# Performance work log

Hardware: AMD Instinct MI355X
Metric: run time of the kernel (lower is better)

The kernel has to match this reference:

```python
import jax, jax.numpy as jnp
import numpy as np
from jax import lax

B, N, FEAT, MID, HID, OUT = 128, 36, 2048, 517, 128, 1024
STEPS, TEMP = 3, 1.0


def setup_inputs() -> dict:
    key = jax.random.key(0)
    ks = jax.random.split(key, 10)
    s = 0.02
    return {
        "boxes": jax.random.uniform(ks[0], (B, 4, N), jnp.float32),
        "attention": jax.random.normal(ks[1], (B, N), jnp.float32),
        "features": jax.random.normal(ks[2], (B, N, FEAT), jnp.float32),
        "conv_w": jax.random.normal(ks[3], (MID - 5, FEAT), jnp.float32) * s,
        "conv_b": jnp.zeros((MID - 5,), jnp.float32),
        "skew_wx": jax.random.normal(ks[4], (HID, MID), jnp.float32) * s,
        "skew_wy": jax.random.normal(ks[5], (HID, MID), jnp.float32) * s,
        "skew_b1": jnp.zeros((HID,), jnp.float32),
        "skew_w2": jax.random.normal(ks[6], (HID,), jnp.float32) * s,
        "skew_b2": jnp.zeros((1,), jnp.float32),
        "w_ih": jax.random.normal(ks[7], (4 * OUT, MID), jnp.float32) * s,
        "w_hh": jax.random.normal(ks[8], (4 * OUT, OUT), jnp.float32) * s,
        "b_ih": jnp.zeros((4 * OUT,), jnp.float32),
        "b_hh": jnp.zeros((4 * OUT,), jnp.float32),
        "lr": jnp.ones((1,), jnp.float32),
    }


def _calculate_assignment(C, lr_abs, temp, steps):
    # C: (b, n, n) skew-symmetric ordering costs.
    logits = jnp.zeros_like(C)
    for _ in range(steps):
        P = jax.nn.softmax(logits / temp, axis=-1)  # position i -> distribution over elements l
        cum = jnp.cumsum(P, axis=1)                 # sum over positions k <= i
        below = cum - P                             # sum_{k<i} P_kl
        above = cum[:, -1:, :] - cum                # sum_{k>i} P_kl
        # grad_{ij} = sum_l C_{jl} * (above - below)_{il}  (uses skew-symmetry of C)
        G = jnp.einsum('bil,bjl->bij', above - below, C)
        logits = logits - lr_abs * G
    return jax.nn.softmax(logits / temp, axis=-1)


def reference(boxes, attention, features, conv_w, conv_b, skew_wx, skew_wy,
              skew_b1, skew_w2, skew_b2, w_ih, w_hh, b_ih, b_hh, lr):
    b = boxes.shape[0]
    # normalize boxes by per-sample max
    boxes = boxes / jnp.max(boxes.reshape(b, -1), axis=1)[:, None, None]
    # pointwise Conv1: 2048 -> MID-5, features arrives as (b, n, 2048)
    f = jnp.einsum('bnf,mf->bmn', features, conv_w) + conv_b[None, :, None]
    att = attention[:, None, :]                      # (b, 1, n)
    feats = jnp.concatenate([boxes, att, f], axis=1)  # (b, MID, n)
    # PairwiseSkew: f(x_i, x_j) - f(x_j, x_i); the first 1x1-conv over concatenated
    # pairs splits into two linear maps so we never materialize (b, 2*MID, n, n).
    hx = jnp.einsum('hm,bmn->bhn', skew_wx, feats)
    hy = jnp.einsum('hm,bmn->bhn', skew_wy, feats)
    h = jax.nn.relu(hx[:, :, :, None] + hy[:, :, None, :] + skew_b1[None, :, None, None])
    out = jnp.einsum('h,bhij->bij', skew_w2, h) + skew_b2[0]  # (b, n, n)
    C = out - jnp.swapaxes(out, 1, 2)  # skew-symmetrize
    A = _calculate_assignment(C, jnp.abs(lr)[0], TEMP, STEPS)
    # gate features by sigmoid(attention) and apply soft permutation
    gated = feats * jax.nn.sigmoid(att)               # (b, MID, n)
    x = jnp.einsum('bcl,bil->bci', gated, A)          # (b, MID, n)
    x_seq = jnp.transpose(x, (2, 0, 1))               # (n, b, MID)
    # single-layer LSTM (PyTorch gate order i, f, g, o); return final cell state
    bias = b_ih + b_hh
    Hd = w_hh.shape[1]
    def step(carry, xt):
        h_, c_ = carry
        gates = xt @ w_ih.T + h_ @ w_hh.T + bias
        i, fg, g, o = jnp.split(gates, 4, axis=-1)
        c_ = jax.nn.sigmoid(fg) * c_ + jax.nn.sigmoid(i) * jnp.tanh(g)
        h_ = jax.nn.sigmoid(o) * jnp.tanh(c_)
        return (h_, c_), None
    init = (jnp.zeros((b, Hd), x.dtype), jnp.zeros((b, Hd), x.dtype))
    (_, c_fin), _ = lax.scan(step, init, x_seq)
    return c_fin
```

## Files before the change

### kernel.cpp

```cpp
#include <hip/hip_runtime.h>
#include <math.h>

#define NB 128
#define NN 36
#define S37 37
#define S40 40
#define NFEAT 2048
#define NMID 517
#define KP 544
#define NHID 128
#define NOUT 1024
#define ROWS (NB*NN)

typedef __bf16 bf16x8 __attribute__((ext_vector_type(8)));
typedef float  f32x4  __attribute__((ext_vector_type(4)));

__device__ __forceinline__ float sigf(float x){ return 1.f/(1.f+expf(-x)); }
__device__ __forceinline__ unsigned short f2bf(float x){
    unsigned u = __float_as_uint(x);
    return (unsigned short)((u + 0x7FFFu + ((u>>16)&1u)) >> 16);
}
__device__ __forceinline__ float bf2f(unsigned short b){
    return __uint_as_float(((unsigned)b) << 16);
}

__global__ __launch_bounds__(256) void prep_all(
    const float* __restrict__ boxes, const float* __restrict__ att,
    const float* __restrict__ features, const float* __restrict__ conv_w,
    const float* __restrict__ wx, const float* __restrict__ wy,
    const float* __restrict__ b1, const float* __restrict__ w_ih,
    const float* __restrict__ w_hh, const float* __restrict__ b_ih,
    const float* __restrict__ b_hh,
    unsigned short* __restrict__ features_bf, unsigned short* __restrict__ convw_bf,
    unsigned short* __restrict__ wxy_bf, float* __restrict__ hxy_b,
    unsigned short* __restrict__ wih_il, unsigned short* __restrict__ whh_il,
    float* __restrict__ comb_b, unsigned short* __restrict__ h0,
    float* __restrict__ c, float* __restrict__ feats)
{
    int gtid = blockIdx.x*256 + threadIdx.x;
    int gs = gridDim.x*256;
    if (gtid < 128*64) {
        int b = gtid >> 6, t = gtid & 63;
        float mx = -1e30f;
        for (int idx = t; idx < 4*NN; idx += 64) mx = fmaxf(mx, boxes[b*4*NN + idx]);
        for (int off = 32; off > 0; off >>= 1) mx = fmaxf(mx, __shfl_down(mx, off));
        mx = __shfl(mx, 0);
        float inv = 1.f / mx;
        for (int idx = t; idx < 4*NN; idx += 64) {
            int r = idx / NN, n = idx - r*NN;
            feats[(size_t)(b*NN+n)*NMID + r] = boxes[b*4*NN + idx] * inv;
        }
        if (t < NN) feats[(size_t)(b*NN+t)*NMID + 4] = att[b*NN + t];
    }
    for (int i = gtid; i < ROWS*NFEAT; i += gs) features_bf[i] = f2bf(features[i]);
    for (int i = gtid; i < 512*NFEAT; i += gs) convw_bf[i] = f2bf(conv_w[i]);
    for (int i = gtid; i < 256*KP; i += gs) {
        int r = i / KP, k = i - r*KP;
        float v = 0.f;
        if (k < NMID) v = (r < NHID) ? wx[(size_t)r*NMID+k] : wy[(size_t)(r-NHID)*NMID+k];
        wxy_bf[i] = f2bf(v);
    }
    for (int i = gtid; i < 256; i += gs) hxy_b[i] = (i < NHID) ? b1[i] : 0.f;
    for (int i = gtid; i < 4*NOUT*KP; i += gs) {
        int row = i / KP, k = i - row*KP;
        int u = row >> 2, g = row & 3;
        wih_il[i] = (k < NMID) ? f2bf(w_ih[(size_t)(g*NOUT+u)*NMID + k]) : (unsigned short)0;
    }
    for (int i = gtid; i < 4*NOUT*NOUT; i += gs) {
        int row = i >> 10, k = i & 1023;
        int u = row >> 2, g = row & 3;
        whh_il[i] = f2bf(w_hh[(size_t)(g*NOUT+u)*NOUT + k]);
    }
    for (int i = gtid; i < 4*NOUT; i += gs) {
        int u = i >> 2, g = i & 3;
        comb_b[i] = b_ih[g*NOUT+u] + b_hh[g*NOUT+u];
    }
    for (int i = gtid; i < NB*NOUT; i += gs) { h0[i] = 0; c[i] = 0.f; }
}

__global__ __launch_bounds__(256) void conv_sk(
    const unsigned short* __restrict__ A, const unsigned short* __restrict__ B,
    float* __restrict__ part)
{
    __shared__ __align__(16) char As[8192];
    __shared__ __align__(16) char Bs[4096];
    int m0 = blockIdx.y * 128, n0 = blockIdx.x * 64;
    int kbeg = blockIdx.z * 512;
    int tid = threadIdx.x;
    int lane = tid & 63, wave = tid >> 6;
    int wm = wave >> 1, wn = wave & 1;
    f32x4 acc[4][2];
    #pragma unroll
    for (int i = 0; i < 4; ++i)
        #pragma unroll
        for (int j = 0; j < 2; ++j) acc[i][j] = (f32x4){0.f,0.f,0.f,0.f};

    for (int k0 = 0; k0 < 512; k0 += 32) {
        #pragma unroll
        for (int cc = tid; cc < 512; cc += 256) {
            int r = cc >> 2, q = cc & 3;
            uint4 v = *(const uint4*)(A + (size_t)(m0+r)*NFEAT + kbeg + k0 + q*8);
            *(uint4*)(As + ((r>>4)<<10) + (q<<8) + ((r&15)<<4)) = v;
        }
        {
            int r = tid >> 2, q = tid & 3;
            uint4 v = *(const uint4*)(B + (size_t)(n0+r)*NFEAT + kbeg + k0 + q*8);
            *(uint4*)(Bs + ((r>>4)<<10) + (q<<8) + ((r&15)<<4)) = v;
        }
        __syncthreads();
        bf16x8 af[4], bfr[2];
        #pragma unroll
        for (int i = 0; i < 4; ++i) af[i]  = *(bf16x8*)(As + ((wm*4+i)<<10) + (lane<<4));
        #pragma unroll
        for (int j = 0; j < 2; ++j) bfr[j] = *(bf16x8*)(Bs + ((wn*2+j)<<10) + (lane<<4));
        #pragma unroll
        for (int i = 0; i < 4; ++i)
            #pragma unroll
            for (int j = 0; j < 2; ++j)
                acc[i][j] = __builtin_amdgcn_mfma_f32_16x16x32_bf16(af[i], bfr[j], acc[i][j], 0, 0, 0);
        __syncthreads();
    }
    float* out = part + (size_t)blockIdx.z * ROWS * 512;
    int colf = lane & 15, rowq = lane >> 4;
    #pragma unroll
    for (int j = 0; j < 2; ++j) {
        int col = n0 + (wn*2+j)*16 + colf;
        #pragma unroll
        for (int i = 0; i < 4; ++i)
            #pragma unroll
            for (int reg = 0; reg < 4; ++reg) {
                int row = m0 + (wm*4+i)*16 + rowq*4 + reg;
                out[(size_t)row*512 + col] = acc[i][j][reg];
            }
    }
}

__global__ __launch_bounds__(256) void conv_reduce(
    const float* __restrict__ part, const float* __restrict__ bias,
    float* __restrict__ feats, unsigned short* __restrict__ feats_bf)
{
    int gtid = blockIdx.x*256 + threadIdx.x;
    int gs = gridDim.x*256;
    const size_t PS = (size_t)ROWS * 512;
    for (int i = gtid; i < ROWS*512; i += gs) {
        int r = i >> 9, cc = i & 511;
        float s = part[i] + part[PS+i] + part[2*PS+i] + part[3*PS+i] + bias[cc];
        feats[(size_t)r*NMID + 5 + cc] = s;
        feats_bf[(size_t)r*KP + 5 + cc] = f2bf(s);
    }
    for (int i = gtid; i < ROWS*5; i += gs) {
        int r = i / 5, cc = i - r*5;
        feats_bf[(size_t)r*KP + cc] = f2bf(feats[(size_t)r*NMID + cc]);
    }
    for (int i = gtid; i < ROWS*27; i += gs) {
        int r = i / 27, cc = i - r*27;
        feats_bf[(size_t)r*KP + 517 + cc] = 0;
    }
}

__global__ __launch_bounds__(256) void gemm_mfma(
    const unsigned short* __restrict__ A, const unsigned short* __restrict__ B,
    const float* __restrict__ bias, void* __restrict__ Cp,
    int K, int lda, int ldb, int ldc, int obf)
{
    __shared__ __align__(16) char As[8192];
    __shared__ __align__(16) char Bs[4096];
    int m0 = blockIdx.y * 128, n0 = blockIdx.x * 64;
    int tid = threadIdx.x;
    int lane = tid & 63, wave = tid >> 6;
    int wm = wave >> 1, wn = wave & 1;
    f32x4 acc[4][2];
    #pragma unroll
    for (int i = 0; i < 4; ++i)
        #pragma unroll
        for (int j = 0; j < 2; ++j) acc[i][j] = (f32x4){0.f,0.f,0.f,0.f};

    for (int k0 = 0; k0 < K; k0 += 32) {
        #pragma unroll
        for (int cc = tid; cc < 512; cc += 256) {
            int r = cc >> 2, q = cc & 3;
            uint4 v = *(const uint4*)(A + (size_t)(m0+r)*lda + k0 + q*8);
            *(uint4*)(As + ((r>>4)<<10) + (q<<8) + ((r&15)<<4)) = v;
        }
        {
            int r = tid >> 2, q = tid & 3;
            uint4 v = *(const uint4*)(B + (size_t)(n0+r)*ldb + k0 + q*8);
            *(uint4*)(Bs + ((r>>4)<<10) + (q<<8) + ((r&15)<<4)) = v;
        }
        __syncthreads();
        bf16x8 af[4], bfr[2];
        #pragma unroll
        for (int i = 0; i < 4; ++i) af[i]  = *(bf16x8*)(As + ((wm*4+i)<<10) + (lane<<4));
        #pragma unroll
        for (int j = 0; j < 2; ++j) bfr[j] = *(bf16x8*)(Bs + ((wn*2+j)<<10) + (lane<<4));
        #pragma unroll
        for (int i = 0; i < 4; ++i)
            #pragma unroll
            for (int j = 0; j < 2; ++j)
                acc[i][j] = __builtin_amdgcn_mfma_f32_16x16x32_bf16(af[i], bfr[j], acc[i][j], 0, 0, 0);
        __syncthreads();
    }
    int colf = lane & 15, rowq = lane >> 4;
    #pragma unroll
    for (int j = 0; j < 2; ++j) {
        int col = n0 + (wn*2+j)*16 + colf;
        float bv = bias ? bias[col] : 0.f;
        #pragma unroll
        for (int i = 0; i < 4; ++i) {
            #pragma unroll
            for (int reg = 0; reg < 4; ++reg) {
                int row = m0 + (wm*4+i)*16 + rowq*4 + reg;
                float v = acc[i][j][reg] + bv;
                if (obf) ((unsigned short*)Cp)[(size_t)row*ldc + col] = f2bf(v);
                else     ((float*)Cp)[(size_t)row*ldc + col] = v;
            }
        }
    }
}

__global__ __launch_bounds__(256) void out_k(
    const float* __restrict__ hxy, const float* __restrict__ w2,
    float* __restrict__ out_g)
{
    __shared__ float s_hx[9*129], s_hy[NN*129], s_w2[NHID];
    int b = blockIdx.x, i0 = blockIdx.y * 9, tid = threadIdx.x;
    for (int i = tid; i < 9*NHID; i += 256) {
        int n = i >> 7, h = i & 127;
        s_hx[n*129+h] = hxy[(size_t)(b*NN+i0+n)*256 + h];
    }
    for (int i = tid; i < NN*NHID; i += 256) {
        int n = i >> 7, h = i & 127;
        s_hy[n*129+h] = hxy[(size_t)(b*NN+n)*256 + 128 + h];
    }
    if (tid < NHID) s_w2[tid] = w2[tid];
    __syncthreads();
    for (int idx = tid; idx < 9*NN; idx += 256) {
        int il = idx / NN, j = idx - il*NN;
        const float* px = &s_hx[il*129];
        const float* py = &s_hy[j*129];
        float s = 0.f;
        #pragma unroll 8
        for (int h = 0; h < NHID; ++h) s += s_w2[h] * fmaxf(px[h] + py[h], 0.f);
        out_g[(size_t)b*NN*NN + (i0+il)*NN + j] = s;
    }
}

__global__ __launch_bounds__(256) void iter_k(
    const float* __restrict__ out_g, const float* __restrict__ att,
    const float* __restrict__ lr, float* __restrict__ A_g)
{
    __shared__ __align__(16) float s_out[NN*S40], s_C[NN*S40], s_logits[NN*S40], s_P[NN*S40];
    __shared__ float s_sg[NN];
    int b = blockIdx.x, tid = threadIdx.x;
    for (int idx = tid; idx < NN*NN; idx += 256) {
        int i = idx / NN, j = idx - i*NN;
        s_out[i*S40+j] = out_g[(size_t)b*NN*NN + idx];
        s_logits[i*S40+j] = 0.f;
    }
    if (tid < NN) s_sg[tid] = sigf(att[b*NN + tid]);
    float lr_abs = fabsf(lr[0]);
    __syncthreads();
    for (int idx = tid; idx < NN*NN; idx += 256) {
        int i = idx / NN, j = idx - i*NN;
        s_C[i*S40+j] = s_out[i*S40+j] - s_out[j*S40+i];
    }
    __syncthreads();
    for (int it = 0; it < 3; ++it) {
        if (tid < NN) {
            int i = tid;
            float mx = -1e30f;
            for (int l = 0; l < NN; ++l) mx = fmaxf(mx, s_logits[i*S40+l]);
            float sum = 0.f;
            for (int l = 0; l < NN; ++l) { float e = expf(s_logits[i*S40+l]-mx); s_P[i*S40+l] = e; sum += e; }
            float inv = 1.f/sum;
            for (int l = 0; l < NN; ++l) s_P[i*S40+l] *= inv;
        }
        __syncthreads();
        if (tid < NN) {
            int l = tid;
            float S = 0.f;
            for (int i = 0; i < NN; ++i) S += s_P[i*S40+l];
            float cum = 0.f;
            for (int i = 0; i < NN; ++i) {
                float p = s_P[i*S40+l];
                cum += p;
                s_P[i*S40+l] = S - 2.f*cum + p;
            }
        }
        __syncthreads();
        for (int idx = tid; idx < NN*NN; idx += 256) {
            int i = idx / NN, j = idx - i*NN;
            const f32x4* Pp = (const f32x4*)&s_P[i*S40];
            const f32x4* Cc = (const f32x4*)&s_C[j*S40];
            float g = 0.f;
            #pragma unroll
            for (int q = 0; q < 9; ++q) {
                f32x4 a = Pp[q], bb = Cc[q];
                g += a[0]*bb[0] + a[1]*bb[1] + a[2]*bb[2] + a[3]*bb[3];
            }
            s_logits[i*S40+j] -= lr_abs * g;
        }
        __syncthreads();
    }
    if (tid < NN) {
        int i = tid;
        float mx = -1e30f;
        for (int l = 0; l < NN; ++l) mx = fmaxf(mx, s_logits[i*S40+l]);
        float sum = 0.f;
        for (int l = 0; l < NN; ++l) { float e = expf(s_logits[i*S40+l]-mx); s_P[i*S40+l] = e; sum += e; }
        float inv = 1.f/sum;
        for (int l = 0; l < NN; ++l)
            A_g[(size_t)b*NN*NN + i*NN + l] = s_P[i*S40+l] * inv * s_sg[l];
    }
}

__global__ __launch_bounds__(256) void xseq_k(
    const float* __restrict__ feats, const float* __restrict__ A_g,
    unsigned short* __restrict__ xseq)
{
    __shared__ float s_P[NN*S37];
    int b = blockIdx.x, half = blockIdx.y, tid = threadIdx.x;
    for (int idx = tid; idx < NN*NN; idx += 256) {
        int i = idx / NN, l = idx - i*NN;
        s_P[i*S37+l] = A_g[(size_t)b*NN*NN + idx];
    }
    __syncthreads();
    const float* fb = feats + (size_t)b*NN*NMID;
    int ncols = (half == 0 && tid < 32) ? 2 : 1;
    #pragma unroll
    for (int rep = 0; rep < 2; ++rep) {
        if (rep >= ncols) break;
        int c = (rep == 0) ? half*256 + tid : 512 + tid;
        float colv[NN];
        #pragma unroll
        for (int l = 0; l < NN; ++l) colv[l] = (c < NMID) ? fb[l*NMID + c] : 0.f;
        #pragma unroll 4
        for (int i = 0; i < NN; ++i) {
            float s = 0.f;
            #pragma unroll
            for (int l = 0; l < NN; ++l) s += s_P[i*S37+l] * colv[l];
            xseq[((size_t)i*NB + b)*KP + c] = f2bf(s);
        }
    }
}

__global__ __launch_bounds__(256) void lstm_step(
    const unsigned short* __restrict__ h_in, const unsigned short* __restrict__ whh,
    const unsigned short* __restrict__ xw_t, float* __restrict__ c,
    unsigned short* __restrict__ h_out, float* __restrict__ cout)
{
    __shared__ __align__(16) char Bls[131072];
    __shared__ float gates[32][68];
    int tid = threadIdx.x, lane = tid & 63, wave = tid >> 6;
    int blk = blockIdx.x;
    int m0 = (blk >> 6) * 32;
    int n0 = (blk & 63) * 64;
    #pragma unroll
    for (int r = 0; r < 32; ++r) {
        int idx = r*256 + tid;
        int kc = idx >> 6, n = idx & 63;
        uint4 v = *(const uint4*)(whh + (size_t)(n0+n)*NOUT + kc*8);
        *(uint4*)(Bls + kc*1024 + n*16) = v;
    }
    __syncthreads();
    int wm = wave & 1, wn = wave >> 1;
    const char* bbase = Bls + (lane>>4)*1024 + wn*512 + (lane&15)*16;
    const unsigned short* hrow = h_in + (size_t)(m0 + wm*16 + (lane&15))*NOUT + (lane>>4)*8;
    f32x4 acc0 = (f32x4){0.f,0.f,0.f,0.f};
    f32x4 acc1 = (f32x4){0.f,0.f,0.f,0.f};
    #pragma unroll 8
    for (int k0 = 0; k0 < NOUT; k0 += 32) {
        bf16x8 a  = *(const bf16x8*)(hrow + k0);
        bf16x8 b0 = *(const bf16x8*)(bbase + (k0<<7));
        bf16x8 b1 = *(const bf16x8*)(bbase + (k0<<7) + 256);
        acc0 = __builtin_amdgcn_mfma_f32_16x16x32_bf16(a, b0, acc0, 0, 0, 0);
        acc1 = __builtin_amdgcn_mfma_f32_16x16x32_bf16(a, b1, acc1, 0, 0, 0);
    }
    int colf = lane & 15, rowq = lane >> 4;
    #pragma unroll
    for (int reg = 0; reg < 4; ++reg) {
        gates[wm*16 + rowq*4 + reg][wn*32 + colf]      = acc0[reg];
        gates[wm*16 + rowq*4 + reg][wn*32 + 16 + colf] = acc1[reg];
    }
    __syncthreads();
    #pragma unroll
    for (int p = 0; p < 2; ++p) {
        int idx = p*256 + tid;
        int ul = idx & 15, bl = idx >> 4;
        int b = m0 + bl, u = (n0 >> 2) + ul;
        float4 gl = *(const float4*)&gates[bl][ul*4];
        uint2 xw2 = *(const uint2*)(xw_t + (size_t)b*4*NOUT + n0 + ul*4);
        float g0 = gl.x + bf2f((unsigned short)(xw2.x & 0xffffu));
        float g1 = gl.y + bf2f((unsigned short)(xw2.x >> 16));
        float g2 = gl.z + bf2f((unsigned short)(xw2.y & 0xffffu));
        float g3 = gl.w + bf2f((unsigned short)(xw2.y >> 16));
        float ig = sigf(g0), fg = sigf(g1), gg = tanhf(g2), og = sigf(g3);
        size_t o = (size_t)b*NOUT + u;
        float cc = fg*c[o] + ig*gg;
        c[o] = cc;
        if (cout) cout[o] = cc;
        else      h_out[o] = f2bf(og*tanhf(cc));
    }
}

extern "C" void kernel_launch(void* const* d_in, const int* in_sizes, int n_in,
                              void* d_out, int out_size, void* d_ws, size_t ws_size,
                              hipStream_t stream) {
    (void)in_sizes; (void)n_in; (void)out_size; (void)ws_size;
    const float* boxes     = (const float*)d_in[0];
    const float* attention = (const float*)d_in[1];
    const float* features  = (const float*)d_in[2];
    const float* conv_w    = (const float*)d_in[3];
    const float* conv_b    = (const float*)d_in[4];
    const float* skew_wx   = (const float*)d_in[5];
    const float* skew_wy   = (const float*)d_in[6];
    const float* skew_b1   = (const float*)d_in[7];
    const float* skew_w2   = (const float*)d_in[8];
    const float* w_ih      = (const float*)d_in[10];
    const float* w_hh      = (const float*)d_in[11];
    const float* b_ih      = (const float*)d_in[12];
    const float* b_hh      = (const float*)d_in[13];
    const float* lr        = (const float*)d_in[14];

    char* ws = (char*)d_ws;
    float*          part     = (float*)(ws);
    unsigned short* xw_bf    = (unsigned short*)(ws);
    unsigned short* features_bf = (unsigned short*)(ws + 37748736);
    unsigned short* convw_bf = (unsigned short*)(ws + 56623104);
    float*          feats    = (float*)(ws + 58720256);
    float*          hxy      = (float*)(ws + 68249600);
    unsigned short* feats_bf = (unsigned short*)(ws + 72968192);
    unsigned short* xseq_bf  = (unsigned short*)(ws + 77981696);
    unsigned short* wih_il   = (unsigned short*)(ws + 82995200);
    unsigned short* whh_il   = (unsigned short*)(ws + 87451648);
    unsigned short* wxy_bf   = (unsigned short*)(ws + 95840256);
    float*          comb_b   = (float*)(ws + 96118784);
    float*          hxy_b    = (float*)(ws + 96135168);
    unsigned short* h0       = (unsigned short*)(ws + 96136192);
    unsigned short* h1       = (unsigned short*)(ws + 96398336);
    float*          out_g    = (float*)(ws + 96660480);
    float*          A_g      = (float*)(ws + 97324032);
    float*          cst      = (float*)(ws + 97987584);

    prep_all<<<2048, 256, 0, stream>>>(boxes, attention, features, conv_w,
                                       skew_wx, skew_wy, skew_b1, w_ih, w_hh,
                                       b_ih, b_hh, features_bf, convw_bf,
                                       wxy_bf, hxy_b, wih_il, whh_il, comb_b,
                                       h0, cst, feats);
    conv_sk<<<dim3(8, 36, 4), 256, 0, stream>>>(features_bf, convw_bf, part);
    conv_reduce<<<2048, 256, 0, stream>>>(part, conv_b, feats, feats_bf);
    gemm_mfma<<<dim3(4, 36), 256, 0, stream>>>(feats_bf, wxy_bf, hxy_b,
                                               (void*)hxy, KP, KP, KP, 256, 0);
    out_k<<<dim3(NB, 4), 256, 0, stream>>>(hxy, skew_w2, out_g);
    iter_k<<<NB, 256, 0, stream>>>(out_g, attention, lr, A_g);
    xseq_k<<<dim3(NB, 2), 256, 0, stream>>>(feats, A_g, xseq_bf);
    gemm_mfma<<<dim3(64, 36), 256, 0, stream>>>(xseq_bf, wih_il, comb_b,
                                                (void*)xw_bf, KP, KP, KP, 4*NOUT, 1);
    unsigned short* hbuf[2] = {h0, h1};
    for (int t = 0; t < NN; ++t) {
        float* co = (t == NN-1) ? (float*)d_out : nullptr;
        lstm_step<<<256, 256, 0, stream>>>(hbuf[t & 1], whh_il,
                                           xw_bf + (size_t)t*NB*4*NOUT, cst,
                                           hbuf[(t+1) & 1], co);
    }
}
```

Baseline: 756.6 us.

## Generalize conv GEMM to 128x128 swizzled tile and halve LSTM step tiles

Replaces the conv split-K kernel with a generic 128x128-tile MFMA GEMM that uses an XOR-swizzled LDS layout, an optional bias, and either bf16 or strided fp32 output. The input-projection GEMM now also uses it. The LSTM step kernel uses 32x32 output tiles with 64KB of LDS and a swizzled W_hh layout, launching 512 blocks with two blocks allowed per CU. The aim is more operand reuse in the GEMMs, fewer LDS bank conflicts, and more parallelism per recurrent step, at the cost of higher register pressure and W_hh being reloaded by more blocks.

```diff
diff --git a/kernel.cpp b/kernel.cpp
--- a/kernel.cpp
+++ b/kernel.cpp
@@ -78,60 +78,64 @@
     for (int i = gtid; i < NB*NOUT; i += gs) { h0[i] = 0; c[i] = 0.f; }
 }
 
-__global__ __launch_bounds__(256) void conv_sk(
+__global__ __launch_bounds__(256) void gemm128(
     const unsigned short* __restrict__ A, const unsigned short* __restrict__ B,
-    float* __restrict__ part)
-{
-    __shared__ __align__(16) char As[8192];
-    __shared__ __align__(16) char Bs[4096];
-    int m0 = blockIdx.y * 128, n0 = blockIdx.x * 64;
-    int kbeg = blockIdx.z * 512;
+    const float* __restrict__ bias, void* __restrict__ Cp,
+    int Ksl, int lda, int ldb, int ldc, int obf, long long pstride)
+{
+    __shared__ __align__(16) char As[16384];
+    __shared__ __align__(16) char Bs[16384];
+    int m0 = blockIdx.y * 128, n0 = blockIdx.x * 128;
+    int kbeg = blockIdx.z * Ksl;
     int tid = threadIdx.x;
     int lane = tid & 63, wave = tid >> 6;
     int wm = wave >> 1, wn = wave & 1;
-    f32x4 acc[4][2];
+    int sw = ((lane>>4)<<8) + (((lane&15) ^ ((lane>>4)<<2))<<4);
+    f32x4 acc[4][4];
     #pragma unroll
     for (int i = 0; i < 4; ++i)
         #pragma unroll
-        for (int j = 0; j < 2; ++j) acc[i][j] = (f32x4){0.f,0.f,0.f,0.f};
-
-    for (int k0 = 0; k0 < 512; k0 += 32) {
-        #pragma unroll
-        for (int cc = tid; cc < 512; cc += 256) {
+        for (int j = 0; j < 4; ++j) acc[i][j] = (f32x4){0.f,0.f,0.f,0.f};
+
+    for (int k0 = 0; k0 < Ksl; k0 += 32) {
+        #pragma unroll
+        for (int p = 0; p < 2; ++p) {
+            int cc = p*256 + tid;
             int r = cc >> 2, q = cc & 3;
-            uint4 v = *(const uint4*)(A + (size_t)(m0+r)*NFEAT + kbeg + k0 + q*8);
-            *(uint4*)(As + ((r>>4)<<10) + (q<<8) + ((r&15)<<4)) = v;
-        }
-        {
-            int r = tid >> 2, q = tid & 3;
-            uint4 v = *(const uint4*)(B + (size_t)(n0+r)*NFEAT + kbeg + k0 + q*8);
-            *(uint4*)(Bs + ((r>>4)<<10) + (q<<8) + ((r&15)<<4)) = v;
-        }
-        __syncthreads();
-        bf16x8 af[4], bfr[2];
-        #pragma unroll
-        for (int i = 0; i < 4; ++i) af[i]  = *(bf16x8*)(As + ((wm*4+i)<<10) + (lane<<4));
-        #pragma unroll
-        for (int j = 0; j < 2; ++j) bfr[j] = *(bf16x8*)(Bs + ((wn*2+j)<<10) + (lane<<4));
+            int sa = ((r>>4)<<10) + (q<<8) + ((((r&15) ^ (q<<2)))<<4);
+            uint4 va = *(const uint4*)(A + (size_t)(m0+r)*lda + kbeg + k0 + q*8);
+            *(uint4*)(As + sa) = va;
+            uint4 vb = *(const uint4*)(B + (size_t)(n0+r)*ldb + kbeg + k0 + q*8);
+            *(uint4*)(Bs + sa) = vb;
+        }
+        __syncthreads();
+        bf16x8 af[4], bfr[4];
+        #pragma unroll
+        for (int i = 0; i < 4; ++i) af[i]  = *(bf16x8*)(As + ((wm*4+i)<<10) + sw);
+        #pragma unroll
+        for (int j = 0; j < 4; ++j) bfr[j] = *(bf16x8*)(Bs + ((wn*4+j)<<10) + sw);
         #pragma unroll
         for (int i = 0; i < 4; ++i)
             #pragma unroll
-            for (int j = 0; j < 2; ++j)
+            for (int j = 0; j < 4; ++j)
                 acc[i][j] = __builtin_amdgcn_mfma_f32_16x16x32_bf16(af[i], bfr[j], acc[i][j], 0, 0, 0);
         __syncthreads();
     }
-    float* out = part + (size_t)blockIdx.z * ROWS * 512;
     int colf = lane & 15, rowq = lane >> 4;
     #pragma unroll
-    for (int j = 0; j < 2; ++j) {
-        int col = n0 + (wn*2+j)*16 + colf;
-        #pragma unroll
-        for (int i = 0; i < 4; ++i)
+    for (int j = 0; j < 4; ++j) {
+        int col = n0 + (wn*4+j)*16 + colf;
+        float bv = bias ? bias[col] : 0.f;
+        #pragma unroll
+        for (int i = 0; i < 4; ++i) {
             #pragma unroll
             for (int reg = 0; reg < 4; ++reg) {
                 int row = m0 + (wm*4+i)*16 + rowq*4 + reg;
-                out[(size_t)row*512 + col] = acc[i][j][reg];
+                float v = acc[i][j][reg] + bv;
+                if (obf) ((unsigned short*)Cp)[(size_t)row*ldc + col] = f2bf(v);
+                else ((float*)Cp + (size_t)blockIdx.z*pstride)[(size_t)row*ldc + col] = v;
             }
+        }
     }
 }
 
@@ -344,50 +348,43 @@
     }
 }
 
-__global__ __launch_bounds__(256) void lstm_step(
+__global__ __launch_bounds__(256, 2) void lstm_step(
     const unsigned short* __restrict__ h_in, const unsigned short* __restrict__ whh,
     const unsigned short* __restrict__ xw_t, float* __restrict__ c,
     unsigned short* __restrict__ h_out, float* __restrict__ cout)
 {
-    __shared__ __align__(16) char Bls[131072];
-    __shared__ float gates[32][68];
+    __shared__ __align__(16) char Bls[65536];
+    __shared__ __align__(16) float gates[32][36];
     int tid = threadIdx.x, lane = tid & 63, wave = tid >> 6;
-    int blk = blockIdx.x;
-    int m0 = (blk >> 6) * 32;
-    int n0 = (blk & 63) * 64;
-    #pragma unroll
-    for (int r = 0; r < 32; ++r) {
+    int bt = blockIdx.x >> 7, ct = blockIdx.x & 127;
+    int m0 = bt * 32, n0 = ct * 32;
+    #pragma unroll
+    for (int r = 0; r < 16; ++r) {
         int idx = r*256 + tid;
-        int kc = idx >> 6, n = idx & 63;
+        int n = idx >> 7, kc = idx & 127;
         uint4 v = *(const uint4*)(whh + (size_t)(n0+n)*NOUT + kc*8);
-        *(uint4*)(Bls + kc*1024 + n*16) = v;
-    }
-    __syncthreads();
-    int wm = wave & 1, wn = wave >> 1;
-    const char* bbase = Bls + (lane>>4)*1024 + wn*512 + (lane&15)*16;
-    const unsigned short* hrow = h_in + (size_t)(m0 + wm*16 + (lane&15))*NOUT + (lane>>4)*8;
-    f32x4 acc0 = (f32x4){0.f,0.f,0.f,0.f};
-    f32x4 acc1 = (f32x4){0.f,0.f,0.f,0.f};
+        *(uint4*)(Bls + kc*512 + (((n&16) | ((n^kc)&15))<<4)) = v;
+    }
+    __syncthreads();
+    int wm = wave >> 1, wn = wave & 1;
+    int q = lane >> 4, ml = lane & 15;
+    const unsigned short* hrow = h_in + (size_t)(m0 + wm*16 + ml)*NOUT + q*8;
+    int nl = wn*16 + ml;
+    f32x4 acc = (f32x4){0.f,0.f,0.f,0.f};
     #pragma unroll 8
-    for (int k0 = 0; k0 < NOUT; k0 += 32) {
-        bf16x8 a  = *(const bf16x8*)(hrow + k0);
-        bf16x8 b0 = *(const bf16x8*)(bbase + (k0<<7));
-        bf16x8 b1 = *(const bf16x8*)(bbase + (k0<<7) + 256);
-        acc0 = __builtin_amdgcn_mfma_f32_16x16x32_bf16(a, b0, acc0, 0, 0, 0);
-        acc1 = __builtin_amdgcn_mfma_f32_16x16x32_bf16(a, b1, acc1, 0, 0, 0);
-    }
-    int colf = lane & 15, rowq = lane >> 4;
-    #pragma unroll
-    for (int reg = 0; reg < 4; ++reg) {
-        gates[wm*16 + rowq*4 + reg][wn*32 + colf]      = acc0[reg];
-        gates[wm*16 + rowq*4 + reg][wn*32 + 16 + colf] = acc1[reg];
-    }
-    __syncthreads();
-    #pragma unroll
-    for (int p = 0; p < 2; ++p) {
-        int idx = p*256 + tid;
-        int ul = idx & 15, bl = idx >> 4;
-        int b = m0 + bl, u = (n0 >> 2) + ul;
+    for (int it = 0; it < 32; ++it) {
+        int kc = it*4 + q;
+        bf16x8 a = *(const bf16x8*)(hrow + it*32);
+        bf16x8 b = *(const bf16x8*)(Bls + kc*512 + (((nl&16) | ((nl^kc)&15))<<4));
+        acc = __builtin_amdgcn_mfma_f32_16x16x32_bf16(a, b, acc, 0, 0, 0);
+    }
+    #pragma unroll
+    for (int reg = 0; reg < 4; ++reg)
+        gates[wm*16 + q*4 + reg][wn*16 + ml] = acc[reg];
+    __syncthreads();
+    {
+        int ul = tid & 7, bl = tid >> 3;
+        int b = m0 + bl, u = ct*8 + ul;
         float4 gl = *(const float4*)&gates[bl][ul*4];
         uint2 xw2 = *(const uint2*)(xw_t + (size_t)b*4*NOUT + n0 + ul*4);
         float g0 = gl.x + bf2f((unsigned short)(xw2.x & 0xffffu));
@@ -447,19 +444,21 @@
                                        b_ih, b_hh, features_bf, convw_bf,
                                        wxy_bf, hxy_b, wih_il, whh_il, comb_b,
                                        h0, cst, feats);
-    conv_sk<<<dim3(8, 36, 4), 256, 0, stream>>>(features_bf, convw_bf, part);
+    gemm128<<<dim3(4, 36, 4), 256, 0, stream>>>(features_bf, convw_bf, nullptr,
+                                                (void*)part, 512, NFEAT, NFEAT, 512, 0,
+                                                (long long)ROWS*512);
     conv_reduce<<<2048, 256, 0, stream>>>(part, conv_b, feats, feats_bf);
     gemm_mfma<<<dim3(4, 36), 256, 0, stream>>>(feats_bf, wxy_bf, hxy_b,
                                                (void*)hxy, KP, KP, KP, 256, 0);
     out_k<<<dim3(NB, 4), 256, 0, stream>>>(hxy, skew_w2, out_g);
     iter_k<<<NB, 256, 0, stream>>>(out_g, attention, lr, A_g);
     xseq_k<<<dim3(NB, 2), 256, 0, stream>>>(feats, A_g, xseq_bf);
-    gemm_mfma<<<dim3(64, 36), 256, 0, stream>>>(xseq_bf, wih_il, comb_b,
-                                                (void*)xw_bf, KP, KP, KP, 4*NOUT, 1);
+    gemm128<<<dim3(32, 36, 1), 256, 0, stream>>>(xseq_bf, wih_il, comb_b,
+                                                 (void*)xw_bf, KP, KP, KP, 4*NOUT, 1, 0);
     unsigned short* hbuf[2] = {h0, h1};
     for (int t = 0; t < NN; ++t) {
         float* co = (t == NN-1) ? (float*)d_out : nullptr;
-        lstm_step<<<256, 256, 0, stream>>>(hbuf[t & 1], whh_il,
+        lstm_step<<<512, 256, 0, stream>>>(hbuf[t & 1], whh_il,
                                            xw_bf + (size_t)t*NB*4*NOUT, cst,
                                            hbuf[(t+1) & 1], co);
     }
```

After: 708.4 us. 1.07x faster.
